# Performance work log

Hardware: AMD Instinct MI355X
Metric: run time of the kernel (lower is better)

Reference implementation:

```python
import jax, jax.numpy as jnp
import numpy as np

# Static window half-sizes derived from the init sigma values (~2.5*sigma),
# matching the sigma-dependent window of the MONAI trainable bilateral filter CUDA kernel.
KX = 2
KY = 2


def setup_inputs() -> dict:
    key = jax.random.key(0)
    x = jax.random.normal(key, (16, 1, 1024, 1024), dtype=jnp.float32)
    return {
        "x": x,
        "sigma_x": jnp.float32(1.0),
        "sigma_y": jnp.float32(1.0),
        "sigma_z": jnp.float32(1.0),
        "sigma_color": jnp.float32(0.5),
    }


def reference(x, sigma_x, sigma_y, sigma_z, sigma_color):
    # x: [B, 1, H, W] (z-dim is singleton after the module's unsqueeze, so only
    # the dz=0 tap exists; its spatial weight factor is exp(0)=1).
    B, C, H, W = x.shape
    inv2sx = 1.0 / (2.0 * sigma_x * sigma_x)
    inv2sy = 1.0 / (2.0 * sigma_y * sigma_y)
    inv2sz = 1.0 / (2.0 * sigma_z * sigma_z)
    inv2sr = 1.0 / (2.0 * sigma_color * sigma_color)

    xp = jnp.pad(x, ((0, 0), (0, 0), (KX, KX), (KY, KY)))
    mp = jnp.pad(jnp.ones_like(x), ((0, 0), (0, 0), (KX, KX), (KY, KY)))

    num = jnp.zeros_like(x)
    den = jnp.zeros_like(x)
    dz = 0  # singleton z dimension -> only the center tap
    for dx in range(-KX, KX + 1):
        for dy in range(-KY, KY + 1):
            xs = xp[:, :, KX + dx:KX + dx + H, KY + dy:KY + dy + W]
            ms = mp[:, :, KX + dx:KX + dx + H, KY + dy:KY + dy + W]
            diff = x - xs
            w = ms * jnp.exp(-(dx * dx) * inv2sx - (dy * dy) * inv2sy
                             - (dz * dz) * inv2sz - diff * diff * inv2sr)
            num = num + w * xs
            den = den + w
    return num / den
```

## Files before the change

kernel.cpp:

```cpp
#include <hip/hip_runtime.h>
#include <math.h>

#if __has_builtin(__builtin_amdgcn_exp2f)
#define EXP2F(x) __builtin_amdgcn_exp2f(x)
#else
#define EXP2F(x) exp2f(x)
#endif
#if __has_builtin(__builtin_amdgcn_rcpf)
#define RCPF(x) __builtin_amdgcn_rcpf(x)
#else
#define RCPF(x) (1.0f / (x))
#endif

namespace {
constexpr int IMG  = 1024;
constexpr int TW   = 64;
constexpr int TH   = 16;
constexpr int LDSW = 72;
constexpr int LDSH = TH + 4;
constexpr float BIG   = 1e18f;
constexpr float LOG2E = 1.4426950408889634f;
constexpr float K1     = 0.84932180028801907f;
constexpr float INV_K1 = 1.17741002251547466f;
}

__global__ __launch_bounds__(256)
void bilateral5x5(const float* __restrict__ x,
                  const float* __restrict__ p_sx,
                  const float* __restrict__ p_sy,
                  const float* __restrict__ p_sr,
                  float* __restrict__ out)
{
    __shared__ float tile[LDSH * LDSW];

    const int tx  = threadIdx.x;
    const int ty  = threadIdx.y;
    const int tid = ty * 16 + tx;

    const int gx0 = blockIdx.x * TW - 2;
    const int gy0 = blockIdx.y * TH - 2;
    const float* img = x + (size_t)blockIdx.z * (IMG * IMG);

    const float srv   = p_sr[0];
    const float s     = K1 / srv;
    const float inv_s = srv * INV_K1;

    for (int idx = tid; idx < LDSH * 68; idx += 256) {
        const int r  = idx / 68;
        const int c  = idx - r * 68;
        const int gx = gx0 + c;
        const int gy = gy0 + r;
        float v = BIG;
        if ((unsigned)gx < (unsigned)IMG && (unsigned)gy < (unsigned)IMG)
            v = img[gy * IMG + gx] * s;
        tile[r * LDSW + c] = v;
    }
    __syncthreads();

    const float sxv = p_sx[0], syv = p_sy[0];
    const float ax  = -LOG2E / (2.0f * sxv * sxv);
    const float ay  = -LOG2E / (2.0f * syv * syv);
    float lsx[5], lsy[5];
    #pragma unroll
    for (int j = 0; j < 5; ++j) {
        const float dj = (float)((j - 2) * (j - 2));
        lsx[j] = ax * dj;
        lsy[j] = ay * dj;
    }

    const int base = tx * 4;
    float num[4] = {0.f, 0.f, 0.f, 0.f};
    float den[4] = {0.f, 0.f, 0.f, 0.f};
    float ctr[4];
    {
        const float4 a = *reinterpret_cast<const float4*>(&tile[(ty + 2) * LDSW + base]);
        const float4 b = *reinterpret_cast<const float4*>(&tile[(ty + 2) * LDSW + base + 4]);
        ctr[0] = a.z; ctr[1] = a.w; ctr[2] = b.x; ctr[3] = b.y;
    }

    #pragma unroll
    for (int dy = 0; dy < 5; ++dy) {
        const float4 a = *reinterpret_cast<const float4*>(&tile[(ty + dy) * LDSW + base]);
        const float4 b = *reinterpret_cast<const float4*>(&tile[(ty + dy) * LDSW + base + 4]);
        const float v[8] = {a.x, a.y, a.z, a.w, b.x, b.y, b.z, b.w};
        #pragma unroll
        for (int dx = 0; dx < 5; ++dx) {
            const float ls = lsy[dy] + lsx[dx];
            #pragma unroll
            for (int i = 0; i < 4; ++i) {
                const float us = v[i + dx];
                const float d  = ctr[i] - us;
                const float w  = EXP2F(fmaf(-d, d, ls));
                num[i] = fmaf(w, us, num[i]);
                den[i] += w;
            }
        }
    }

    float* outimg = out + (size_t)blockIdx.z * (IMG * IMG);
    const int oy = blockIdx.y * TH + ty;
    const int ox = blockIdx.x * TW + tx * 4;
    float4 o;
    o.x = num[0] * RCPF(den[0]) * inv_s;
    o.y = num[1] * RCPF(den[1]) * inv_s;
    o.z = num[2] * RCPF(den[2]) * inv_s;
    o.w = num[3] * RCPF(den[3]) * inv_s;
    *reinterpret_cast<float4*>(&outimg[oy * IMG + ox]) = o;
}

extern "C" void kernel_launch(void* const* d_in, const int* in_sizes, int n_in,
                              void* d_out, int out_size, void* d_ws, size_t ws_size,
                              hipStream_t stream) {
    const float* x  = (const float*)d_in[0];
    const float* sx = (const float*)d_in[1];
    const float* sy = (const float*)d_in[2];
    const float* sr = (const float*)d_in[4];
    float* out = (float*)d_out;

    const int B = in_sizes[0] / (IMG * IMG);
    dim3 grid(IMG / TW, IMG / TH, B);
    dim3 block(16, 16, 1);
    bilateral5x5<<<grid, block, 0, stream>>>(x, sx, sy, sr, out);
}
```

Before: 180.1 us.

## Exploit weight symmetry and compute 4x4 outputs per thread with larger tiles

Each thread now computes a 4x4 block of outputs over a 64x64 tile. Pairs of pixels that both lie inside the thread's block share one exp evaluation, since the bilateral weight is symmetric. The centre tap is seeded directly as weight 1. This cuts the number of exp evaluations and the LDS reads per output, and enlarges the tile to shrink the halo overhead. The cost is higher register pressure (48 accumulators, with a launch bound of 4 blocks) and a larger LDS footprint, which lowers occupancy.

```diff
diff --git a/kernel.cpp b/kernel.cpp
--- a/kernel.cpp
+++ b/kernel.cpp
@@ -15,16 +15,16 @@
 namespace {
 constexpr int IMG  = 1024;
 constexpr int TW   = 64;
-constexpr int TH   = 16;
-constexpr int LDSW = 72;
-constexpr int LDSH = TH + 4;
+constexpr int TH   = 64;
+constexpr int LDSW = 68;
+constexpr int LDSH = 68;
 constexpr float BIG   = 1e18f;
 constexpr float LOG2E = 1.4426950408889634f;
 constexpr float K1     = 0.84932180028801907f;
 constexpr float INV_K1 = 1.17741002251547466f;
 }
 
-__global__ __launch_bounds__(256)
+__global__ __launch_bounds__(256, 4)
 void bilateral5x5(const float* __restrict__ x,
                   const float* __restrict__ p_sx,
                   const float* __restrict__ p_sy,
@@ -45,67 +45,89 @@
     const float s     = K1 / srv;
     const float inv_s = srv * INV_K1;
 
-    for (int idx = tid; idx < LDSH * 68; idx += 256) {
-        const int r  = idx / 68;
-        const int c  = idx - r * 68;
+    for (int idx = tid; idx < LDSH * LDSW; idx += 256) {
+        const int r  = idx / LDSW;
+        const int c  = idx - r * LDSW;
         const int gx = gx0 + c;
         const int gy = gy0 + r;
         float v = BIG;
         if ((unsigned)gx < (unsigned)IMG && (unsigned)gy < (unsigned)IMG)
             v = img[gy * IMG + gx] * s;
-        tile[r * LDSW + c] = v;
+        tile[idx] = v;
     }
     __syncthreads();
 
     const float sxv = p_sx[0], syv = p_sy[0];
-    const float ax  = -LOG2E / (2.0f * sxv * sxv);
-    const float ay  = -LOG2E / (2.0f * syv * syv);
-    float lsx[5], lsy[5];
+    const float ar = -LOG2E / (2.0f * sxv * sxv);
+    const float ac = -LOG2E / (2.0f * syv * syv);
+    float ls9[3][3];
     #pragma unroll
-    for (int j = 0; j < 5; ++j) {
-        const float dj = (float)((j - 2) * (j - 2));
-        lsx[j] = ax * dj;
-        lsy[j] = ay * dj;
-    }
+    for (int i = 0; i < 3; ++i)
+        #pragma unroll
+        for (int j = 0; j < 3; ++j)
+            ls9[i][j] = ar * (float)(i * i) + ac * (float)(j * j);
 
-    const int base = tx * 4;
-    float num[4] = {0.f, 0.f, 0.f, 0.f};
-    float den[4] = {0.f, 0.f, 0.f, 0.f};
-    float ctr[4];
-    {
-        const float4 a = *reinterpret_cast<const float4*>(&tile[(ty + 2) * LDSW + base]);
-        const float4 b = *reinterpret_cast<const float4*>(&tile[(ty + 2) * LDSW + base + 4]);
-        ctr[0] = a.z; ctr[1] = a.w; ctr[2] = b.x; ctr[3] = b.y;
+    const float4* t4 = reinterpret_cast<const float4*>(tile);
+    const int r0 = ty * 4;
+
+    float c[4][4], num[4][4], den[4][4];
+    #pragma unroll
+    for (int r = 0; r < 4; ++r) {
+        const int lr = r0 + 2 + r;
+        const float4 a = t4[lr * 17 + tx];
+        const float4 b = t4[lr * 17 + tx + 1];
+        c[r][0] = a.z; c[r][1] = a.w; c[r][2] = b.x; c[r][3] = b.y;
+        #pragma unroll
+        for (int j = 0; j < 4; ++j) { num[r][j] = c[r][j]; den[r][j] = 1.0f; }
     }
 
     #pragma unroll
-    for (int dy = 0; dy < 5; ++dy) {
-        const float4 a = *reinterpret_cast<const float4*>(&tile[(ty + dy) * LDSW + base]);
-        const float4 b = *reinterpret_cast<const float4*>(&tile[(ty + dy) * LDSW + base + 4]);
+    for (int wr = 0; wr < 8; ++wr) {
+        const int lr = r0 + wr;
+        const float4 a = t4[lr * 17 + tx];
+        const float4 b = t4[lr * 17 + tx + 1];
         const float v[8] = {a.x, a.y, a.z, a.w, b.x, b.y, b.z, b.w};
         #pragma unroll
-        for (int dx = 0; dx < 5; ++dx) {
-            const float ls = lsy[dy] + lsx[dx];
+        for (int orow = 0; orow < 4; ++orow) {
+            const int dy = wr - 2 - orow;
+            if (dy < -2 || dy > 2) continue;
+            const int ady = dy < 0 ? -dy : dy;
             #pragma unroll
-            for (int i = 0; i < 4; ++i) {
-                const float us = v[i + dx];
-                const float d  = ctr[i] - us;
-                const float w  = EXP2F(fmaf(-d, d, ls));
-                num[i] = fmaf(w, us, num[i]);
-                den[i] += w;
+            for (int ocol = 0; ocol < 4; ++ocol) {
+                #pragma unroll
+                for (int dx = -2; dx <= 2; ++dx) {
+                    if (dy == 0 && dx == 0) continue;
+                    const int wc  = ocol + 2 + dx;
+                    const int adx = dx < 0 ? -dx : dx;
+                    const bool qown = (wr >= 2 && wr <= 5 && wc >= 2 && wc <= 5);
+                    if (qown && (dy < 0 || (dy == 0 && dx < 0))) continue;
+                    const float u = v[wc];
+                    const float d = c[orow][ocol] - u;
+                    const float w = EXP2F(fmaf(-d, d, ls9[ady][adx]));
+                    num[orow][ocol] = fmaf(w, u, num[orow][ocol]);
+                    den[orow][ocol] += w;
+                    if (qown) {
+                        const int qr = wr - 2, qc = wc - 2;
+                        num[qr][qc] = fmaf(w, c[orow][ocol], num[qr][qc]);
+                        den[qr][qc] += w;
+                    }
+                }
             }
         }
     }
 
     float* outimg = out + (size_t)blockIdx.z * (IMG * IMG);
-    const int oy = blockIdx.y * TH + ty;
-    const int ox = blockIdx.x * TW + tx * 4;
-    float4 o;
-    o.x = num[0] * RCPF(den[0]) * inv_s;
-    o.y = num[1] * RCPF(den[1]) * inv_s;
-    o.z = num[2] * RCPF(den[2]) * inv_s;
-    o.w = num[3] * RCPF(den[3]) * inv_s;
-    *reinterpret_cast<float4*>(&outimg[oy * IMG + ox]) = o;
+    const int gxo = blockIdx.x * TW + tx * 4;
+    #pragma unroll
+    for (int r = 0; r < 4; ++r) {
+        const int gy = blockIdx.y * TH + ty * 4 + r;
+        float4 o;
+        o.x = num[r][0] * RCPF(den[r][0]) * inv_s;
+        o.y = num[r][1] * RCPF(den[r][1]) * inv_s;
+        o.z = num[r][2] * RCPF(den[r][2]) * inv_s;
+        o.w = num[r][3] * RCPF(den[r][3]) * inv_s;
+        *reinterpret_cast<float4*>(&outimg[gy * IMG + gxo]) = o;
+    }
 }
 
 extern "C" void kernel_launch(void* const* d_in, const int* in_sizes, int n_in,
```

Measured after the change: 280.4 us. 1.56x slower.
